# Kernel optimization log

Hardware: AMD Instinct MI355X
Metric: run time of the kernel (lower is better)

Reference implementation:

```python
import jax, jax.numpy as jnp
import numpy as np

H, W, C = 2048, 2048, 8
N = 4_194_304


def setup_inputs() -> dict:
    key = jax.random.key(0)
    k1, k2 = jax.random.split(key, 2)
    coords = jax.random.uniform(k1, (N, 2), jnp.float32, 0.0, float(H - 1))
    visible = jax.random.normal(k2, (H, W, C), jnp.float32)
    bias = jnp.zeros((2,), jnp.float32)
    return {"coords": coords, "visible": visible, "bias": bias}


def _interp(idx, visible):
    # Faithful translation of linear_interpolation forward.
    hw = jnp.asarray(visible.shape[:-1], jnp.float32)  # [H, W]
    c = jnp.maximum(idx, 0.0)
    low = jnp.minimum(jnp.floor(c), hw - 2.0)
    delta = c - low                                     # [N, 2]
    i = low.astype(jnp.int32)
    i0, i1 = i[:, 0], i[:, 1]
    tl = visible[i0,     i1]       # idx_low
    tr = visible[i0 + 1, i1]       # idx_low + [1, 0]
    bl = visible[i0,     i1 + 1]   # idx_low + [0, 1]
    br = visible[i0 + 1, i1 + 1]   # idx_low + [1, 1]
    d0 = delta[:, :1]   # delta along first axis, broadcast over channels
    d1 = delta[:, 1:2]  # delta along second axis
    mid_bottom = br + d0 * (bl - br)
    mid_top    = tr + d0 * (tl - tr)
    interp = mid_bottom + d1 * (mid_top - mid_bottom)   # [N, C]
    return interp


def reference(coords, visible, bias):
    idx = coords.astype(jnp.float32) - bias
    return _interp(idx, visible)
```

## Files before the change

kernel.cpp:

```cpp
#include <hip/hip_runtime.h>

#define IMG_H 2048
#define IMG_W 2048
#define IMG_C 8

typedef float f32x2 __attribute__((ext_vector_type(2)));
typedef float f32x4 __attribute__((ext_vector_type(4)));

__global__ __launch_bounds__(256) void idx2pixel_kernel(
    const float* __restrict__ coords,
    const float* __restrict__ visible,
    const float* __restrict__ bias,
    float* __restrict__ out,
    int n)
{
    int tid = blockIdx.x * blockDim.x + threadIdx.x;
    int s    = tid >> 1;
    int part = tid & 1;
    if (s >= n) return;

    f32x2 cv = __builtin_nontemporal_load((const f32x2*)(coords + (size_t)s * 2));
    float b0 = bias[0];
    float b1 = bias[1];

    float c0 = fmaxf(cv.x - b0, 0.0f);
    float c1 = fmaxf(cv.y - b1, 0.0f);
    float low0 = fminf(floorf(c0), (float)(IMG_H - 2));
    float low1 = fminf(floorf(c1), (float)(IMG_W - 2));
    float d0 = c0 - low0;
    float d1 = c1 - low1;
    int i0 = (int)low0;
    int i1 = (int)low1;

    const float* p_t = visible + ((size_t)i0 * IMG_W + (size_t)i1) * IMG_C + part * 4;
    const float* p_b = p_t + (size_t)IMG_W * IMG_C;

    float4 tl = *(const float4*)(p_t);
    float4 bl = *(const float4*)(p_t + 8);
    float4 tr = *(const float4*)(p_b);
    float4 br = *(const float4*)(p_b + 8);

    f32x4 o;
    {
        float mb, mt;
        mb = br.x + d0 * (bl.x - br.x); mt = tr.x + d0 * (tl.x - tr.x);
        o.x = mb + d1 * (mt - mb);
        mb = br.y + d0 * (bl.y - br.y); mt = tr.y + d0 * (tl.y - tr.y);
        o.y = mb + d1 * (mt - mb);
        mb = br.z + d0 * (bl.z - br.z); mt = tr.z + d0 * (tl.z - tr.z);
        o.z = mb + d1 * (mt - mb);
        mb = br.w + d0 * (bl.w - br.w); mt = tr.w + d0 * (tl.w - tr.w);
        o.w = mb + d1 * (mt - mb);
    }

    __builtin_nontemporal_store(o, (f32x4*)(out + (size_t)s * IMG_C + part * 4));
}

extern "C" void kernel_launch(void* const* d_in, const int* in_sizes, int n_in,
                              void* d_out, int out_size, void* d_ws, size_t ws_size,
                              hipStream_t stream) {
    const float* coords  = (const float*)d_in[0];
    const float* visible = (const float*)d_in[1];
    const float* bias    = (const float*)d_in[2];
    float* out = (float*)d_out;

    int n = in_sizes[0] / 2;
    long long threads = 2LL * n;
    int block = 256;
    long long grid = (threads + block - 1) / block;
    idx2pixel_kernel<<<(int)grid, block, 0, stream>>>(coords, visible, bias, out, n);
}
```

Baseline: 398.7 us.

## Bin samples by row slab before gathering to improve image cache locality

```diff
diff --git a/kernel.cpp b/kernel.cpp
--- a/kernel.cpp
+++ b/kernel.cpp
@@ -4,10 +4,149 @@
 #define IMG_W 2048
 #define IMG_C 8
 
-typedef float f32x2 __attribute__((ext_vector_type(2)));
-typedef float f32x4 __attribute__((ext_vector_type(4)));
-
-__global__ __launch_bounds__(256) void idx2pixel_kernel(
+#define KBINS      64
+#define SLAB_SHIFT 5
+#define SPT        16
+#define SBLOCK     256
+
+__device__ __forceinline__ float4 lerp4(float4 tl, float4 tr, float4 bl, float4 br,
+                                        float d0, float d1) {
+    float4 o;
+    float mb, mt;
+    mb = br.x + d0 * (bl.x - br.x); mt = tr.x + d0 * (tl.x - tr.x); o.x = mb + d1 * (mt - mb);
+    mb = br.y + d0 * (bl.y - br.y); mt = tr.y + d0 * (tl.y - tr.y); o.y = mb + d1 * (mt - mb);
+    mb = br.z + d0 * (bl.z - br.z); mt = tr.z + d0 * (tl.z - tr.z); o.z = mb + d1 * (mt - mb);
+    mb = br.w + d0 * (bl.w - br.w); mt = tr.w + d0 * (tl.w - tr.w); o.w = mb + d1 * (mt - mb);
+    return o;
+}
+
+__global__ __launch_bounds__(SBLOCK) void scatter_kernel(
+    const float* __restrict__ coords,
+    const float* __restrict__ visible,
+    const float* __restrict__ bias,
+    float* __restrict__ out,
+    unsigned* __restrict__ cursor,
+    unsigned* __restrict__ recIdx,
+    float* __restrict__ recX,
+    float* __restrict__ recY,
+    int n, unsigned cap)
+{
+    __shared__ unsigned hist[KBINS];
+    __shared__ unsigned basev[KBINS];
+    __shared__ unsigned lofs[KBINS];
+
+    int t = threadIdx.x;
+    if (t < KBINS) hist[t] = 0;
+    __syncthreads();
+
+    int blockStart = blockIdx.x * (SBLOCK * SPT);
+    float b0 = bias[0];
+    float b1 = bias[1];
+
+    for (int k = 0; k < SPT; ++k) {
+        int s = blockStart + k * SBLOCK + t;
+        if (s < n) {
+            float cx = coords[2 * (size_t)s];
+            float c0 = fmaxf(cx - b0, 0.0f);
+            float low0 = fminf(floorf(c0), (float)(IMG_H - 2));
+            int i0 = (int)low0;
+            atomicAdd(&hist[i0 >> SLAB_SHIFT], 1u);
+        }
+    }
+    __syncthreads();
+
+    if (t < KBINS) {
+        basev[t] = atomicAdd(&cursor[t], hist[t]);
+        lofs[t] = 0;
+    }
+    __syncthreads();
+
+    for (int k = 0; k < SPT; ++k) {
+        int s = blockStart + k * SBLOCK + t;
+        if (s < n) {
+            float2 cv = *(const float2*)(coords + 2 * (size_t)s);
+            float c0 = fmaxf(cv.x - b0, 0.0f);
+            float low0 = fminf(floorf(c0), (float)(IMG_H - 2));
+            int i0 = (int)low0;
+            int b = i0 >> SLAB_SHIFT;
+            unsigned off = atomicAdd(&lofs[b], 1u);
+            unsigned slot = basev[b] + off;
+            if (slot < cap) {
+                size_t g = (size_t)b * cap + slot;
+                recIdx[g] = (unsigned)s;
+                recX[g] = cv.x;
+                recY[g] = cv.y;
+            } else {
+                float c1 = fmaxf(cv.y - b1, 0.0f);
+                float low1 = fminf(floorf(c1), (float)(IMG_W - 2));
+                float d0 = c0 - low0;
+                float d1 = c1 - low1;
+                int i1 = (int)low1;
+                const float* pt = visible + ((size_t)i0 * IMG_W + (size_t)i1) * IMG_C;
+                const float* pb = pt + (size_t)IMG_W * IMG_C;
+                for (int q = 0; q < 2; ++q) {
+                    float4 tl = *(const float4*)(pt + 4 * q);
+                    float4 bl = *(const float4*)(pt + 8 + 4 * q);
+                    float4 tr = *(const float4*)(pb + 4 * q);
+                    float4 br = *(const float4*)(pb + 8 + 4 * q);
+                    float4 o = lerp4(tl, tr, bl, br, d0, d1);
+                    *(float4*)(out + (size_t)s * IMG_C + 4 * q) = o;
+                }
+            }
+        }
+    }
+}
+
+__global__ __launch_bounds__(256) void gather_kernel(
+    const float* __restrict__ visible,
+    const float* __restrict__ bias,
+    const unsigned* __restrict__ cursor,
+    const unsigned* __restrict__ recIdx,
+    const float* __restrict__ recX,
+    const float* __restrict__ recY,
+    float* __restrict__ out,
+    unsigned cap, unsigned long long magicM)
+{
+    unsigned tid = blockIdx.x * blockDim.x + threadIdx.x;
+    unsigned j = tid >> 1;
+    unsigned part = tid & 1;
+    if (j >= (unsigned)KBINS * cap) return;
+
+    unsigned b = (unsigned)(((unsigned long long)j * magicM) >> 40);
+    unsigned pos = j - b * cap;
+    unsigned cnt = cursor[b];
+    cnt = cnt > cap ? cap : cnt;
+    if (pos >= cnt) return;
+
+    unsigned s = recIdx[j];
+    float cx = recX[j];
+    float cy = recY[j];
+    float b0 = bias[0];
+    float b1 = bias[1];
+
+    float c0 = fmaxf(cx - b0, 0.0f);
+    float c1 = fmaxf(cy - b1, 0.0f);
+    float low0 = fminf(floorf(c0), (float)(IMG_H - 2));
+    float low1 = fminf(floorf(c1), (float)(IMG_W - 2));
+    float d0 = c0 - low0;
+    float d1 = c1 - low1;
+    int i0 = (int)low0;
+    int i1 = (int)low1;
+
+    const float* p_t = visible + ((size_t)i0 * IMG_W + (size_t)i1) * IMG_C + part * 4;
+    const float* p_b = p_t + (size_t)IMG_W * IMG_C;
+
+    float4 tl = *(const float4*)(p_t);
+    float4 bl = *(const float4*)(p_t + 8);
+    float4 tr = *(const float4*)(p_b);
+    float4 br = *(const float4*)(p_b + 8);
+
+    float4 o = lerp4(tl, tr, bl, br, d0, d1);
+
+    *(float4*)(out + (size_t)s * IMG_C + part * 4) = o;
+}
+
+__global__ __launch_bounds__(256) void idx2pixel_simple(
     const float* __restrict__ coords,
     const float* __restrict__ visible,
     const float* __restrict__ bias,
@@ -15,11 +154,11 @@
     int n)
 {
     int tid = blockIdx.x * blockDim.x + threadIdx.x;
-    int s    = tid >> 1;
+    int s = tid >> 1;
     int part = tid & 1;
     if (s >= n) return;
 
-    f32x2 cv = __builtin_nontemporal_load((const f32x2*)(coords + (size_t)s * 2));
+    float2 cv = *(const float2*)(coords + 2 * (size_t)s);
     float b0 = bias[0];
     float b1 = bias[1];
 
@@ -40,20 +179,8 @@
     float4 tr = *(const float4*)(p_b);
     float4 br = *(const float4*)(p_b + 8);
 
-    f32x4 o;
-    {
-        float mb, mt;
-        mb = br.x + d0 * (bl.x - br.x); mt = tr.x + d0 * (tl.x - tr.x);
-        o.x = mb + d1 * (mt - mb);
-        mb = br.y + d0 * (bl.y - br.y); mt = tr.y + d0 * (tl.y - tr.y);
-        o.y = mb + d1 * (mt - mb);
-        mb = br.z + d0 * (bl.z - br.z); mt = tr.z + d0 * (tl.z - tr.z);
-        o.z = mb + d1 * (mt - mb);
-        mb = br.w + d0 * (bl.w - br.w); mt = tr.w + d0 * (tl.w - tr.w);
-        o.w = mb + d1 * (mt - mb);
-    }
-
-    __builtin_nontemporal_store(o, (f32x4*)(out + (size_t)s * IMG_C + part * 4));
+    float4 o = lerp4(tl, tr, bl, br, d0, d1);
+    *(float4*)(out + (size_t)s * IMG_C + part * 4) = o;
 }
 
 extern "C" void kernel_launch(void* const* d_in, const int* in_sizes, int n_in,
@@ -65,8 +192,33 @@
     float* out = (float*)d_out;
 
     int n = in_sizes[0] / 2;
-    long long threads = 2LL * n;
-    int block = 256;
-    long long grid = (threads + block - 1) / block;
-    idx2pixel_kernel<<<(int)grid, block, 0, stream>>>(coords, visible, bias, out, n);
-}
+    if (n <= 0) return;
+
+    unsigned cap = (unsigned)((unsigned long long)n / KBINS * 106ull / 100ull + 1024ull);
+    size_t need = 256 + (size_t)KBINS * cap * 12;
+
+    if (ws_size < need) {
+        long long threads = 2LL * n;
+        int block = 256;
+        long long grid = (threads + block - 1) / block;
+        idx2pixel_simple<<<(int)grid, block, 0, stream>>>(coords, visible, bias, out, n);
+        return;
+    }
+
+    unsigned* cursor = (unsigned*)d_ws;
+    unsigned* recIdx = (unsigned*)((char*)d_ws + 256);
+    float* recX = (float*)(recIdx + (size_t)KBINS * cap);
+    float* recY = recX + (size_t)KBINS * cap;
+
+    hipMemsetAsync(cursor, 0, KBINS * sizeof(unsigned), stream);
+
+    int sblocks = (n + SBLOCK * SPT - 1) / (SBLOCK * SPT);
+    scatter_kernel<<<sblocks, SBLOCK, 0, stream>>>(
+        coords, visible, bias, out, cursor, recIdx, recX, recY, n, cap);
+
+    unsigned long long magicM = ((1ull << 40) + cap - 1) / cap;
+    long long threads = 2LL * KBINS * (long long)cap;
+    int gblocks = (int)((threads + 255) / 256);
+    gather_kernel<<<gblocks, 256, 0, stream>>>(
+        visible, bias, cursor, recIdx, recX, recY, out, cap, magicM);
+}
```

Result: slower. 472.4 us (+18.5%).
